# Performance work log

Hardware: AMD Instinct MI355X
Metric: run time of the kernel (lower is better)

The kernel has to match this reference:

```python
import jax, jax.numpy as jnp
import numpy as np

N = 100000
E = 3200000
IN, HID, OUT = 512, 256, 64
K = 10
ALPHA = 0.1


def setup_inputs() -> dict:
    key = jax.random.key(0)
    ks = jax.random.split(key, 8)
    x = jax.random.normal(ks[0], (N, IN), dtype=jnp.float32)
    edge_index = jax.random.randint(ks[1], (2, E), 0, N, dtype=jnp.int64)
    W1 = jax.random.normal(ks[2], (IN, HID), dtype=jnp.float32) / np.sqrt(IN)
    b1 = jnp.zeros((HID,), dtype=jnp.float32)
    W2 = jax.random.normal(ks[3], (HID, OUT), dtype=jnp.float32) / np.sqrt(HID)
    b2 = jnp.zeros((OUT,), dtype=jnp.float32)
    # PPR init: temp[k] = alpha*(1-alpha)^k, temp[K] = (1-alpha)^K
    temp = ALPHA * (1.0 - ALPHA) ** np.arange(K + 1)
    temp[-1] = (1.0 - ALPHA) ** K
    temp = jnp.asarray(temp, dtype=jnp.float32)
    return {"x": x, "edge_index": edge_index, "W1": W1, "b1": b1,
            "W2": W2, "b2": b2, "temp": temp}


def reference(x, edge_index, W1, b1, W2, b2, temp):
    n = x.shape[0]
    # MLP (dropout = identity in eval mode)
    h = jax.nn.relu(x @ W1 + b1) @ W2 + b2  # [N, OUT]

    # gcn_norm: add self-loops, edge_weight = 1, sym-normalize
    loops = jnp.arange(n, dtype=edge_index.dtype)
    row = jnp.concatenate([edge_index[0], loops])  # source (x_j)
    col = jnp.concatenate([edge_index[1], loops])  # target (aggregate into)
    w = jnp.ones(row.shape[0], dtype=h.dtype)
    deg = jax.ops.segment_sum(w, col, num_segments=n)
    dinv = jnp.where(deg > 0, jax.lax.rsqrt(deg), 0.0)
    norm = dinv[row] * w * dinv[col]  # [E+N]

    hidden = h * temp[0]

    def step(carry, gamma):
        cur, hid = carry
        msg = norm[:, None] * cur[row]                       # gather+scale
        cur = jax.ops.segment_sum(msg, col, num_segments=n)  # scatter-add
        hid = hid + gamma * cur
        return (cur, hid), None

    (_, hidden), _ = jax.lax.scan(step, (h, hidden), temp[1:])
    return hidden
```

## Files before the change

kernel.cpp:

```cpp
#include <hip/hip_runtime.h>
#include <hip/hip_bf16.h>

#define NN   100000
#define EE   3200000
#define INF  512
#define HIDF 256
#define OUTF 64
#define KSTEPS 10

typedef __attribute__((ext_vector_type(8))) short short8;
typedef __attribute__((ext_vector_type(4))) float floatx4;
typedef unsigned short ushort_t;

static __device__ inline short bf2s(__hip_bfloat16 h) {
    return __builtin_bit_cast(short, h);
}

static __device__ inline unsigned short f2bf(float f) {
    unsigned u = __float_as_uint(f);
    unsigned r = (u + 0x7FFFu + ((u >> 16) & 1u)) >> 16;
    return (unsigned short)r;
}

static __device__ inline float b2f(unsigned short u) {
    return __uint_as_float(((unsigned)u) << 16);
}


__global__ void zero_kernel(int* p, int n) {
    int i = blockIdx.x * 256 + threadIdx.x;
    if (i < n) p[i] = 0;
}

__global__ void count_kernel(const int* __restrict__ ei, int* __restrict__ counts) {
    int e = blockIdx.x * 256 + threadIdx.x;
    if (e < EE) atomicAdd(&counts[ei[EE + e]], 1);
}

__global__ void dinv_kernel(const int* __restrict__ counts, float* __restrict__ dinv) {
    int i = blockIdx.x * 256 + threadIdx.x;
    if (i < NN) dinv[i] = rsqrtf((float)(counts[i] + 1));
}

__global__ void scan1(const int* __restrict__ counts, int* __restrict__ offs,
                      int* __restrict__ partial) {
    __shared__ int s[256];
    int tid = threadIdx.x;
    int i = blockIdx.x * 256 + tid;
    int v = (i < NN) ? counts[i] : 0;
    s[tid] = v;
    __syncthreads();
    for (int d = 1; d < 256; d <<= 1) {
        int t = (tid >= d) ? s[tid - d] : 0;
        __syncthreads();
        s[tid] += t;
        __syncthreads();
    }
    if (i < NN) offs[i] = s[tid] - v;
    if (tid == 255) partial[blockIdx.x] = s[255];
}

__global__ void scan2(int* partial, int nblocks) {
    __shared__ int s[512];
    int tid = threadIdx.x;
    int v = (tid < nblocks) ? partial[tid] : 0;
    s[tid] = v;
    __syncthreads();
    for (int d = 1; d < 512; d <<= 1) {
        int t = (tid >= d) ? s[tid - d] : 0;
        __syncthreads();
        s[tid] += t;
        __syncthreads();
    }
    if (tid < nblocks) partial[tid] = s[tid] - v;
}

__global__ void scan3(int* __restrict__ offs, const int* __restrict__ partial) {
    int i = blockIdx.x * 256 + threadIdx.x;
    if (i < NN) offs[i] += partial[i >> 8];
    else if (i == NN) offs[NN] = EE;
}

__global__ void fill_kernel(const int* __restrict__ ei, const int* __restrict__ offs,
                            int* __restrict__ counts, int* __restrict__ srcIdx) {
    int e = blockIdx.x * 256 + threadIdx.x;
    if (e >= EE) return;
    int r = ei[e];
    int c = ei[EE + e];
    int old = atomicSub(&counts[c], 1);
    srcIdx[offs[c] + old - 1] = r;
}

__global__ void pack_w1(const float* __restrict__ W1, short* __restrict__ W1p) {
    int id = blockIdx.x * 256 + threadIdx.x;
    if (id >= INF * HIDF) return;
    int jj = id & 7, l = (id >> 3) & 15, q = (id >> 7) & 3, t = (id >> 9) & 15, kk = id >> 13;
    int k = kk * 32 + q * 8 + jj, n = t * 16 + l;
    W1p[id] = (short)f2bf(W1[k * HIDF + n]);
}

__global__ void pack_w2(const float* __restrict__ W2, short* __restrict__ W2p) {
    int id = blockIdx.x * 256 + threadIdx.x;
    if (id >= HIDF * OUTF) return;
    int jj = id & 7, l = (id >> 3) & 15, q = (id >> 7) & 3, t = (id >> 9) & 3, kk = id >> 11;
    int k = kk * 32 + q * 8 + jj, n = t * 16 + l;
    W2p[id] = (short)f2bf(W2[k * OUTF + n]);
}


__global__ __launch_bounds__(256) void mlp_kernel(
    const float* __restrict__ x, const short* __restrict__ W1p,
    const short* __restrict__ W2p, const float* __restrict__ b1,
    const float* __restrict__ b2, const float* __restrict__ temp,
    const float* __restrict__ dinv,
    ushort_t* __restrict__ z0, float* __restrict__ out) {

    __shared__ __align__(16) short hlds[64][HIDF + 8];

    int tid = threadIdx.x;
    int wave = tid >> 6, lane = tid & 63;
    int l16 = lane & 15, quad = lane >> 4;
    int brow = blockIdx.x * 64;

    const floatx4 zf = {0.f, 0.f, 0.f, 0.f};
    floatx4 acc[4][4];
#pragma unroll
    for (int mi = 0; mi < 4; mi++)
#pragma unroll
        for (int j = 0; j < 4; j++) acc[mi][j] = zf;

    const float* rp[4];
#pragma unroll
    for (int mi = 0; mi < 4; mi++) {
        int row = brow + mi * 16 + l16;
        if (row > NN - 1) row = NN - 1;
        rp[mi] = x + (size_t)row * INF + quad * 8;
    }

    for (int kk = 0; kk < 16; kk++) {
        short8 a[4];
#pragma unroll
        for (int mi = 0; mi < 4; mi++) {
            const float4* ap = reinterpret_cast<const float4*>(rp[mi] + kk * 32);
            float4 f0 = ap[0];
            float4 f1 = ap[1];
            __hip_bfloat162 q0 = __float22bfloat162_rn(make_float2(f0.x, f0.y));
            __hip_bfloat162 q1 = __float22bfloat162_rn(make_float2(f0.z, f0.w));
            __hip_bfloat162 q2 = __float22bfloat162_rn(make_float2(f1.x, f1.y));
            __hip_bfloat162 q3 = __float22bfloat162_rn(make_float2(f1.z, f1.w));
            short8 av;
            av[0] = bf2s(q0.x); av[1] = bf2s(q0.y);
            av[2] = bf2s(q1.x); av[3] = bf2s(q1.y);
            av[4] = bf2s(q2.x); av[5] = bf2s(q2.y);
            av[6] = bf2s(q3.x); av[7] = bf2s(q3.y);
            a[mi] = av;
        }
        short8 b[4];
#pragma unroll
        for (int j = 0; j < 4; j++) {
            int t = wave * 4 + j;
            b[j] = *reinterpret_cast<const short8*>(
                W1p + (((size_t)(kk * 16 + t) * 64 + quad * 16 + l16) << 3));
        }
#pragma unroll
        for (int mi = 0; mi < 4; mi++)
#pragma unroll
            for (int j = 0; j < 4; j++)
                acc[mi][j] = __builtin_amdgcn_mfma_f32_16x16x32_bf16(a[mi], b[j], acc[mi][j], 0, 0, 0);
    }

#pragma unroll
    for (int j = 0; j < 4; j++) {
        float bj = b1[wave * 64 + j * 16 + l16];
#pragma unroll
        for (int mi = 0; mi < 4; mi++)
#pragma unroll
            for (int r = 0; r < 4; r++) {
                float v = acc[mi][j][r] + bj;
                v = fmaxf(v, 0.f);
                hlds[mi * 16 + quad * 4 + r][wave * 64 + j * 16 + l16] = (short)f2bf(v);
            }
    }
    __syncthreads();

    floatx4 acc2[4];
#pragma unroll
    for (int j = 0; j < 4; j++) acc2[j] = zf;

#pragma unroll
    for (int kk = 0; kk < 8; kk++) {
        short8 a2 = *reinterpret_cast<const short8*>(&hlds[wave * 16 + l16][kk * 32 + quad * 8]);
#pragma unroll
        for (int j = 0; j < 4; j++) {
            short8 bb = *reinterpret_cast<const short8*>(
                W2p + (((size_t)(kk * 4 + j) * 64 + quad * 16 + l16) << 3));
            acc2[j] = __builtin_amdgcn_mfma_f32_16x16x32_bf16(a2, bb, acc2[j], 0, 0, 0);
        }
    }

    float t0 = temp[0];
#pragma unroll
    for (int j = 0; j < 4; j++) {
        float bb = b2[j * 16 + l16];
#pragma unroll
        for (int r = 0; r < 4; r++) {
            int row = brow + wave * 16 + quad * 4 + r;
            if (row < NN) {
                float v = acc2[j][r] + bb;
                size_t o = (size_t)row * 64 + j * 16 + l16;
                out[o] = t0 * v;
                z0[o] = f2bf(dinv[row] * v);
            }
        }
    }
}


#define BLO(u) __uint_as_float((u) << 16)
#define BHI(u) __uint_as_float((u) & 0xFFFF0000u)
#define ACC8(v)                      \
    do {                             \
        a0 += BLO((v).x);            \
        a1 += BHI((v).x);            \
        a2 += BLO((v).y);            \
        a3 += BHI((v).y);            \
        a4 += BLO((v).z);            \
        a5 += BHI((v).z);            \
        a6 += BLO((v).w);            \
        a7 += BHI((v).w);            \
    } while (0)

__global__ __launch_bounds__(256, 8) void prop_kernel(
    const int* __restrict__ srcIdx, const int* __restrict__ offs,
    const float* __restrict__ dinv, const ushort_t* __restrict__ z,
    ushort_t* __restrict__ zn, float* __restrict__ hid,
    const float* __restrict__ temp, int k, int write_z) {

    int node = blockIdx.x * 4 + (threadIdx.x >> 6);
    int lane = threadIdx.x & 63;
    int g = lane >> 3;
    int q = lane & 7;

    int beg = __builtin_amdgcn_readfirstlane(offs[node]);
    int end = __builtin_amdgcn_readfirstlane(offs[node + 1]);

    float a0 = 0.f, a1 = 0.f, a2 = 0.f, a3 = 0.f;
    float a4 = 0.f, a5 = 0.f, a6 = 0.f, a7 = 0.f;

    {
        uint4 v = reinterpret_cast<const uint4*>(z + ((size_t)node << 6))[q];
        if (g == 0) ACC8(v);
    }

    int e = beg;
    for (; e + 16 <= end; e += 16) {
        int s0 = srcIdx[e + g];
        int s1 = srcIdx[e + 8 + g];
        uint4 v0 = reinterpret_cast<const uint4*>(z + ((size_t)s0 << 6))[q];
        uint4 v1 = reinterpret_cast<const uint4*>(z + ((size_t)s1 << 6))[q];
        ACC8(v0);
        ACC8(v1);
    }
    for (; e < end; e += 8) {
        int ee = e + g;
        int cl = (ee < end) ? ee : (end - 1);
        int s = srcIdx[cl];
        uint4 v = reinterpret_cast<const uint4*>(z + ((size_t)s << 6))[q];
        if (ee < end) ACC8(v);
    }

#pragma unroll
    for (int m = 8; m < 64; m <<= 1) {
        a0 += __shfl_xor(a0, m);
        a1 += __shfl_xor(a1, m);
        a2 += __shfl_xor(a2, m);
        a3 += __shfl_xor(a3, m);
        a4 += __shfl_xor(a4, m);
        a5 += __shfl_xor(a5, m);
        a6 += __shfl_xor(a6, m);
        a7 += __shfl_xor(a7, m);
    }

    float dv = dinv[node];
    float tk = temp[k];
    float c0 = dv * a0, c1 = dv * a1, c2 = dv * a2, c3 = dv * a3;
    float c4 = dv * a4, c5 = dv * a5, c6 = dv * a6, c7 = dv * a7;

    if (g == 0) {
        float* hp = hid + ((size_t)node << 6) + q * 8;
        float4 h0 = *reinterpret_cast<float4*>(hp);
        float4 h1 = *reinterpret_cast<float4*>(hp + 4);
        h0.x += tk * c0; h0.y += tk * c1; h0.z += tk * c2; h0.w += tk * c3;
        h1.x += tk * c4; h1.y += tk * c5; h1.z += tk * c6; h1.w += tk * c7;
        *reinterpret_cast<float4*>(hp) = h0;
        *reinterpret_cast<float4*>(hp + 4) = h1;
        if (write_z) {
            uint4 u;
            u.x = (unsigned)f2bf(dv * c0) | ((unsigned)f2bf(dv * c1) << 16);
            u.y = (unsigned)f2bf(dv * c2) | ((unsigned)f2bf(dv * c3) << 16);
            u.z = (unsigned)f2bf(dv * c4) | ((unsigned)f2bf(dv * c5) << 16);
            u.w = (unsigned)f2bf(dv * c6) | ((unsigned)f2bf(dv * c7) << 16);
            reinterpret_cast<uint4*>(zn + ((size_t)node << 6))[q] = u;
        }
    }
}


extern "C" void kernel_launch(void* const* d_in, const int* in_sizes, int n_in,
                              void* d_out, int out_size, void* d_ws, size_t ws_size,
                              hipStream_t stream) {
    const float* x    = (const float*)d_in[0];
    const int*   ei   = (const int*)d_in[1];
    const float* W1   = (const float*)d_in[2];
    const float* b1   = (const float*)d_in[3];
    const float* W2   = (const float*)d_in[4];
    const float* b2   = (const float*)d_in[5];
    const float* temp = (const float*)d_in[6];
    float* out = (float*)d_out;

    char* p = (char*)d_ws;
    auto carve = [&](size_t bytes) -> char* {
        char* r = p;
        p += (bytes + 255) & ~(size_t)255;
        return r;
    };
    ushort_t* zA   = (ushort_t*)carve(sizeof(ushort_t) * (size_t)NN * 64);
    ushort_t* zB   = (ushort_t*)carve(sizeof(ushort_t) * (size_t)NN * 64);
    int* srcIdx    = (int*)carve(sizeof(int) * (size_t)EE);
    int* counts    = (int*)carve(sizeof(int) * NN);
    int* offs      = (int*)carve(sizeof(int) * (NN + 1));
    int* partial   = (int*)carve(sizeof(int) * 512);
    float* dinv    = (float*)carve(sizeof(float) * NN);
    short* W1p     = (short*)carve(sizeof(short) * INF * HIDF);
    short* W2p     = (short*)carve(sizeof(short) * HIDF * OUTF);

    const int NB = (NN + 255) / 256;

    zero_kernel<<<NB, 256, 0, stream>>>(counts, NN);
    pack_w1<<<(INF * HIDF + 255) / 256, 256, 0, stream>>>(W1, W1p);
    pack_w2<<<(HIDF * OUTF + 255) / 256, 256, 0, stream>>>(W2, W2p);

    count_kernel<<<EE / 256, 256, 0, stream>>>(ei, counts);
    dinv_kernel<<<NB, 256, 0, stream>>>(counts, dinv);
    scan1<<<NB, 256, 0, stream>>>(counts, offs, partial);
    scan2<<<1, 512, 0, stream>>>(partial, NB);
    scan3<<<(NN + 256) / 256, 256, 0, stream>>>(offs, partial);
    fill_kernel<<<EE / 256, 256, 0, stream>>>(ei, offs, counts, srcIdx);

    mlp_kernel<<<(NN + 63) / 64, 256, 0, stream>>>(x, W1p, W2p, b1, b2, temp, dinv, zA, out);

    ushort_t* a = zA;
    ushort_t* b = zB;
    for (int k = 1; k <= KSTEPS; k++) {
        prop_kernel<<<NN / 4, 256, 0, stream>>>(srcIdx, offs, dinv, a, b, out, temp, k,
                                                (k < KSTEPS) ? 1 : 0);
        ushort_t* t = a; a = b; b = t;
    }
}
```

Baseline: 1.295 ms.

## Split bf16 feature matrix into column slabs for cache-local SpMM gathers

```diff
diff --git a/kernel.cpp b/kernel.cpp
--- a/kernel.cpp
+++ b/kernel.cpp
@@ -10,6 +10,7 @@
 
 typedef __attribute__((ext_vector_type(8))) short short8;
 typedef __attribute__((ext_vector_type(4))) float floatx4;
+typedef __attribute__((ext_vector_type(4))) float f32x4;
 typedef unsigned short ushort_t;
 
 static __device__ inline short bf2s(__hip_bfloat16 h) {
@@ -207,9 +208,8 @@
             int row = brow + wave * 16 + quad * 4 + r;
             if (row < NN) {
                 float v = acc2[j][r] + bb;
-                size_t o = (size_t)row * 64 + j * 16 + l16;
-                out[o] = t0 * v;
-                z0[o] = f2bf(dinv[row] * v);
+                out[(size_t)row * 64 + j * 16 + l16] = t0 * v;
+                z0[(size_t)j * (NN * 16) + (size_t)row * 16 + l16] = f2bf(dinv[row] * v);
             }
         }
     }
@@ -236,41 +236,51 @@
     ushort_t* __restrict__ zn, float* __restrict__ hid,
     const float* __restrict__ temp, int k, int write_z) {
 
-    int node = blockIdx.x * 4 + (threadIdx.x >> 6);
+    int bid = blockIdx.x;
+    int slab = bid & 3;
+    int chunk = bid >> 2;
     int lane = threadIdx.x & 63;
-    int g = lane >> 3;
-    int q = lane & 7;
-
-    int beg = __builtin_amdgcn_readfirstlane(offs[node]);
-    int end = __builtin_amdgcn_readfirstlane(offs[node + 1]);
+    int wid = threadIdx.x >> 6;
+    int n = lane >> 4;
+    int g = (lane >> 1) & 7;
+    int q = lane & 1;
+
+    int node = chunk * 16 + wid * 4 + n;
+
+    const ushort_t* zs = z + (size_t)slab * (NN * 16);
+
+    int beg = offs[node];
+    int end = offs[node + 1];
 
     float a0 = 0.f, a1 = 0.f, a2 = 0.f, a3 = 0.f;
     float a4 = 0.f, a5 = 0.f, a6 = 0.f, a7 = 0.f;
 
     {
-        uint4 v = reinterpret_cast<const uint4*>(z + ((size_t)node << 6))[q];
+        uint4 v = reinterpret_cast<const uint4*>(zs + (size_t)node * 16)[q];
         if (g == 0) ACC8(v);
     }
 
     int e = beg;
     for (; e + 16 <= end; e += 16) {
-        int s0 = srcIdx[e + g];
-        int s1 = srcIdx[e + 8 + g];
-        uint4 v0 = reinterpret_cast<const uint4*>(z + ((size_t)s0 << 6))[q];
-        uint4 v1 = reinterpret_cast<const uint4*>(z + ((size_t)s1 << 6))[q];
+        int s0 = __builtin_nontemporal_load(srcIdx + e + g);
+        int s1 = __builtin_nontemporal_load(srcIdx + e + 8 + g);
+        uint4 v0 = reinterpret_cast<const uint4*>(zs + (size_t)s0 * 16)[q];
+        uint4 v1 = reinterpret_cast<const uint4*>(zs + (size_t)s1 * 16)[q];
         ACC8(v0);
         ACC8(v1);
     }
     for (; e < end; e += 8) {
         int ee = e + g;
         int cl = (ee < end) ? ee : (end - 1);
-        int s = srcIdx[cl];
-        uint4 v = reinterpret_cast<const uint4*>(z + ((size_t)s << 6))[q];
-        if (ee < end) ACC8(v);
-    }
-
-#pragma unroll
-    for (int m = 8; m < 64; m <<= 1) {
+        int s = __builtin_nontemporal_load(srcIdx + cl);
+        if (ee < end) {
+            uint4 v = reinterpret_cast<const uint4*>(zs + (size_t)s * 16)[q];
+            ACC8(v);
+        }
+    }
+
+#pragma unroll
+    for (int m = 2; m <= 8; m <<= 1) {
         a0 += __shfl_xor(a0, m);
         a1 += __shfl_xor(a1, m);
         a2 += __shfl_xor(a2, m);
@@ -287,20 +297,21 @@
     float c4 = dv * a4, c5 = dv * a5, c6 = dv * a6, c7 = dv * a7;
 
     if (g == 0) {
-        float* hp = hid + ((size_t)node << 6) + q * 8;
-        float4 h0 = *reinterpret_cast<float4*>(hp);
-        float4 h1 = *reinterpret_cast<float4*>(hp + 4);
-        h0.x += tk * c0; h0.y += tk * c1; h0.z += tk * c2; h0.w += tk * c3;
-        h1.x += tk * c4; h1.y += tk * c5; h1.z += tk * c6; h1.w += tk * c7;
-        *reinterpret_cast<float4*>(hp) = h0;
-        *reinterpret_cast<float4*>(hp + 4) = h1;
+        float* hp = hid + (size_t)node * 64 + slab * 16 + q * 8;
+        f32x4 h0 = __builtin_nontemporal_load(reinterpret_cast<f32x4*>(hp));
+        f32x4 h1 = __builtin_nontemporal_load(reinterpret_cast<f32x4*>(hp) + 1);
+        h0[0] += tk * c0; h0[1] += tk * c1; h0[2] += tk * c2; h0[3] += tk * c3;
+        h1[0] += tk * c4; h1[1] += tk * c5; h1[2] += tk * c6; h1[3] += tk * c7;
+        __builtin_nontemporal_store(h0, reinterpret_cast<f32x4*>(hp));
+        __builtin_nontemporal_store(h1, reinterpret_cast<f32x4*>(hp) + 1);
         if (write_z) {
             uint4 u;
             u.x = (unsigned)f2bf(dv * c0) | ((unsigned)f2bf(dv * c1) << 16);
             u.y = (unsigned)f2bf(dv * c2) | ((unsigned)f2bf(dv * c3) << 16);
             u.z = (unsigned)f2bf(dv * c4) | ((unsigned)f2bf(dv * c5) << 16);
             u.w = (unsigned)f2bf(dv * c6) | ((unsigned)f2bf(dv * c7) << 16);
-            reinterpret_cast<uint4*>(zn + ((size_t)node << 6))[q] = u;
+            reinterpret_cast<uint4*>(zn + (size_t)slab * (NN * 16) +
+                                     (size_t)node * 16)[q] = u;
         }
     }
 }
@@ -352,8 +363,8 @@
     ushort_t* a = zA;
     ushort_t* b = zB;
     for (int k = 1; k <= KSTEPS; k++) {
-        prop_kernel<<<NN / 4, 256, 0, stream>>>(srcIdx, offs, dinv, a, b, out, temp, k,
-                                                (k < KSTEPS) ? 1 : 0);
+        prop_kernel<<<(NN / 16) * 4, 256, 0, stream>>>(srcIdx, offs, dinv, a, b, out, temp, k,
+                                                       (k < KSTEPS) ? 1 : 0);
         ushort_t* t = a; a = b; b = t;
     }
 }
```

Result: slower. 1.881 ms (+45.3%).

## Pre-bin edges by destination range before CSR fill to localize atomics

Applied to the files above, without the earlier changes.

```diff
diff --git a/kernel.cpp b/kernel.cpp
--- a/kernel.cpp
+++ b/kernel.cpp
@@ -7,6 +7,9 @@
 #define HIDF 256
 #define OUTF 64
 #define KSTEPS 10
+
+#define NBIN 7
+#define BINSH 14
 
 typedef __attribute__((ext_vector_type(8))) short short8;
 typedef __attribute__((ext_vector_type(4))) float floatx4;
@@ -81,12 +84,61 @@
     else if (i == NN) offs[NN] = EE;
 }
 
-__global__ void fill_kernel(const int* __restrict__ ei, const int* __restrict__ offs,
-                            int* __restrict__ counts, int* __restrict__ srcIdx) {
-    int e = blockIdx.x * 256 + threadIdx.x;
-    if (e >= EE) return;
-    int r = ei[e];
-    int c = ei[EE + e];
+__global__ void init_bins(const int* __restrict__ offs, int* __restrict__ binOffs,
+                          int* __restrict__ cursors) {
+    int t = threadIdx.x;
+    if (t < NBIN + 1) {
+        int v = (t < NBIN) ? offs[t << BINSH] : EE;
+        binOffs[t] = v;
+        if (t < NBIN) cursors[t] = v;
+    }
+}
+
+__global__ __launch_bounds__(256) void bin_kernel(
+    const int* __restrict__ ei, int* __restrict__ cursors,
+    unsigned* __restrict__ packed) {
+    __shared__ int lcount[NBIN];
+    __shared__ int lbase[NBIN];
+    __shared__ unsigned lbuf[NBIN][256];
+    int tid = threadIdx.x;
+    for (int r = blockIdx.x; r < EE / 256; r += gridDim.x) {
+        if (tid < NBIN) lcount[tid] = 0;
+        __syncthreads();
+        int e = r * 256 + tid;
+        int src = ei[e];
+        int c = ei[EE + e];
+        int b = c >> BINSH;
+        int slot = atomicAdd(&lcount[b], 1);
+        lbuf[b][slot] = ((unsigned)src << BINSH) | (unsigned)(c & ((1 << BINSH) - 1));
+        __syncthreads();
+        if (tid < NBIN) lbase[tid] = atomicAdd(&cursors[tid], lcount[tid]);
+        __syncthreads();
+#pragma unroll
+        for (int b2 = 0; b2 < NBIN; b2++) {
+            int n = lcount[b2];
+            int base = lbase[b2];
+            for (int j = tid; j < n; j += 256)
+                packed[base + j] = lbuf[b2][j];
+        }
+        __syncthreads();
+    }
+}
+
+__global__ __launch_bounds__(256) void fill2_kernel(
+    const unsigned* __restrict__ packed, const int* __restrict__ offs,
+    int* __restrict__ counts, int* __restrict__ srcIdx,
+    const int* __restrict__ binOffs) {
+    __shared__ int bo[NBIN + 1];
+    int tid = threadIdx.x;
+    if (tid < NBIN + 1) bo[tid] = binOffs[tid];
+    __syncthreads();
+    int e = blockIdx.x * 256 + tid;
+    int b = 0;
+#pragma unroll
+    for (int i = 1; i < NBIN; i++) b += (e >= bo[i]) ? 1 : 0;
+    unsigned p = packed[e];
+    int c = (b << BINSH) | (int)(p & ((1u << BINSH) - 1));
+    int r = (int)(p >> BINSH);
     int old = atomicSub(&counts[c], 1);
     srcIdx[offs[c] + old - 1] = r;
 }
@@ -333,6 +385,9 @@
     float* dinv    = (float*)carve(sizeof(float) * NN);
     short* W1p     = (short*)carve(sizeof(short) * INF * HIDF);
     short* W2p     = (short*)carve(sizeof(short) * HIDF * OUTF);
+    int* binOffs   = (int*)carve(sizeof(int) * (NBIN + 1));
+    int* cursors   = (int*)carve(sizeof(int) * NBIN);
+    unsigned* packed = (unsigned*)zB;
 
     const int NB = (NN + 255) / 256;
 
@@ -345,7 +400,10 @@
     scan1<<<NB, 256, 0, stream>>>(counts, offs, partial);
     scan2<<<1, 512, 0, stream>>>(partial, NB);
     scan3<<<(NN + 256) / 256, 256, 0, stream>>>(offs, partial);
-    fill_kernel<<<EE / 256, 256, 0, stream>>>(ei, offs, counts, srcIdx);
+
+    init_bins<<<1, 64, 0, stream>>>(offs, binOffs, cursors);
+    bin_kernel<<<1024, 256, 0, stream>>>(ei, cursors, packed);
+    fill2_kernel<<<EE / 256, 256, 0, stream>>>(packed, offs, counts, srcIdx, binOffs);
 
     mlp_kernel<<<(NN + 63) / 64, 256, 0, stream>>>(x, W1p, W2p, b1, b2, temp, dinv, zA, out);
 
```

After: 1.443 ms. 11.5% more time.
